# Kernel tuning notes

Hardware: AMD Instinct MI355X
Metric: run time of the kernel (lower is better)

The kernel has to match this reference:

```python
import jax, jax.numpy as jnp
import numpy as np


def setup_inputs() -> dict:
    key = jax.random.key(0)
    k1, k2, k3 = jax.random.split(key, 3)
    B, T, J, D = 32, 2048, 512, 256
    context = jax.random.normal(k1, (B, T, D), dtype=jnp.float32)
    question = jax.random.normal(k2, (B, J, D), dtype=jnp.float32)
    kernel = jax.random.normal(k3, (3 * D, 1), dtype=jnp.float32) * 0.05
    return {"context": context, "question": question, "kernel": kernel}


def reference(context, question, kernel):
    # Original: tile context to (B,T,J,d), question to (B,T,J,d), concat with
    # elementwise product -> (B,T,J,3d), dot with kernel (3d,1), squeeze.
    # Algebraically identical decomposition (kernel = [wc; wq; wm]):
    #   S[b,t,j] = c[b,t]@wc + q[b,j]@wq + (c[b,t]*wm)@q[b,j]
    D = context.shape[-1]
    w = jnp.squeeze(kernel, axis=-1)          # (3d,)
    wc, wq, wm = w[:D], w[D:2 * D], w[2 * D:]
    c_term = context @ wc                     # (B, T)
    q_term = question @ wq                    # (B, J)
    cross = jnp.einsum('btd,bjd->btj', context * wm, question)  # (B, T, J)
    return cross + c_term[:, :, None] + q_term[:, None, :]
```

## Files before the change

kernel.cpp:

```cpp
#include <hip/hip_runtime.h>
#include <stdint.h>

typedef __bf16 bf16x8 __attribute__((ext_vector_type(8)));
typedef float  f32x4  __attribute__((ext_vector_type(4)));

typedef __attribute__((address_space(1))) const void g_void;
typedef __attribute__((address_space(3))) void l_void;

constexpr int NB = 32, TT = 2048, JJ = 512, DD = 256;
constexpr int CTX_ROWS = NB * TT;
constexpr int QUE_ROWS = NB * JJ;

constexpr size_t WS_QUEB  = 33554432;
constexpr size_t WS_CTERM = 41943040;
constexpr size_t WS_QTERM = 42205184;
constexpr size_t WS_NEED  = 42270720;

__global__ __launch_bounds__(256)
void prep_kernel(const float* __restrict__ ctx, const float* __restrict__ que,
                 const float* __restrict__ wvec,
                 __bf16* __restrict__ ctxb, __bf16* __restrict__ queb,
                 float* __restrict__ cterm, float* __restrict__ qterm)
{
    const int tid  = threadIdx.x;
    const int colg = tid & 31;
    const int rloc = tid >> 5;
    const int k0   = colg * 8;

    const bool isC = (blockIdx.x < 2048);
    const float* src0  = isC ? ctx  : que;
    __bf16*      dst0  = isC ? ctxb : queb;
    float*       term0 = isC ? cterm : qterm;
    const int    rows   = isC ? CTX_ROWS : QUE_ROWS;
    const int    stride = isC ? 2048 * 8 : 512 * 8;
    const int    rg0    = isC ? blockIdx.x : blockIdx.x - 2048;

    const f32x4 wd0 = *(const f32x4*)(wvec + (isC ? 0 : DD) + k0);
    const f32x4 wd1 = *(const f32x4*)(wvec + (isC ? 0 : DD) + k0 + 4);
    f32x4 wm0 = {1.f, 1.f, 1.f, 1.f}, wm1 = {1.f, 1.f, 1.f, 1.f};
    if (isC) { wm0 = *(const f32x4*)(wvec + 2 * DD + k0);
               wm1 = *(const f32x4*)(wvec + 2 * DD + k0 + 4); }

    for (int r = rg0 * 8 + rloc; r < rows; r += stride) {
        const float* src = src0 + (size_t)r * DD + k0;
        const f32x4 x0 = *(const f32x4*)src;
        const f32x4 x1 = *(const f32x4*)(src + 4);

        float d = x0[0]*wd0[0] + x0[1]*wd0[1] + x0[2]*wd0[2] + x0[3]*wd0[3]
                + x1[0]*wd1[0] + x1[1]*wd1[1] + x1[2]*wd1[2] + x1[3]*wd1[3];
        d += __shfl_xor(d, 1);  d += __shfl_xor(d, 2);  d += __shfl_xor(d, 4);
        d += __shfl_xor(d, 8);  d += __shfl_xor(d, 16);

        bf16x8 pk;
        #pragma unroll
        for (int j = 0; j < 4; ++j) {
            pk[j]     = (__bf16)(x0[j] * wm0[j]);
            pk[4 + j] = (__bf16)(x1[j] * wm1[j]);
        }
        *(bf16x8*)(dst0 + (size_t)r * DD + k0) = pk;
        if (colg == 0) term0[r] = d;
    }
}

__global__ __launch_bounds__(256)
void gemm_kernel(const __bf16* __restrict__ ctxb, const __bf16* __restrict__ queb,
                 const float* __restrict__ cterm, const float* __restrict__ qterm,
                 float* __restrict__ out)
{
    __shared__ __align__(1024) unsigned char lds[32768];

    const int tid = threadIdx.x;
    const int l   = tid & 63;
    const int wid = tid >> 6;

    const int pb = blockIdx.x;
    const int id = (pb & 7) * 256 + (pb >> 3);
    const int n0 = (id & 3) * 128;
    const int m0 = ((id >> 2) & 15) * 128;
    const int bI = id >> 6;

    const int lrow8 = l >> 3;
    const int lslot = l & 7;
    const int srcsw = (lslot ^ lrow8) << 3;

    const __bf16* aBase = ctxb + ((size_t)bI * TT + m0 + wid * 32 + lrow8) * DD + srcsw;
    const __bf16* bBase = queb + ((size_t)bI * JJ + n0 + wid * 32 + lrow8) * DD + srcsw;
    unsigned char* ldsA = lds + wid * 4096;
    unsigned char* ldsB = lds + 16384 + wid * 4096;

    auto stage = [&](int k) {
        #pragma unroll
        for (int j = 0; j < 4; ++j) {
            __builtin_amdgcn_global_load_lds((g_void*)(aBase + (size_t)j * 8 * DD + k * 64),
                                             (l_void*)(ldsA + j * 1024), 16, 0, 0);
            __builtin_amdgcn_global_load_lds((g_void*)(bBase + (size_t)j * 8 * DD + k * 64),
                                             (l_void*)(ldsB + j * 1024), 16, 0, 0);
        }
    };

    stage(0);

    f32x4 acc[4][4];
    #pragma unroll
    for (int m = 0; m < 4; ++m)
        #pragma unroll
        for (int n = 0; n < 4; ++n) acc[m][n] = f32x4{0.f, 0.f, 0.f, 0.f};

    const int wm_0 = (wid >> 1) * 64;
    const int wn_0 = (wid & 1) * 64;
    const int lr = l & 15;
    const int hi = l >> 4;

    #pragma unroll
    for (int k = 0; k < 4; ++k) {
        asm volatile("s_waitcnt vmcnt(0)" ::: "memory");
        __builtin_amdgcn_s_barrier();

        bf16x8 af[2][4], bfr[2][4];
        #pragma unroll
        for (int kk = 0; kk < 2; ++kk) {
            const int c = kk * 4 + hi;
            #pragma unroll
            for (int m = 0; m < 4; ++m) {
                const int r = wm_0 + m * 16 + lr;
                af[kk][m] = *(const bf16x8*)(lds + r * 128 + ((c ^ (r & 7)) << 4));
            }
            #pragma unroll
            for (int n = 0; n < 4; ++n) {
                const int r = wn_0 + n * 16 + lr;
                bfr[kk][n] = *(const bf16x8*)(lds + 16384 + r * 128 + ((c ^ (r & 7)) << 4));
            }
        }
        asm volatile("s_waitcnt lgkmcnt(0)" ::: "memory");
        __builtin_amdgcn_sched_barrier(0);
        __builtin_amdgcn_s_barrier();
        if (k < 3) stage(k + 1);

        __builtin_amdgcn_s_setprio(1);
        #pragma unroll
        for (int kk = 0; kk < 2; ++kk)
            #pragma unroll
            for (int m = 0; m < 4; ++m)
                #pragma unroll
                for (int n = 0; n < 4; ++n)
                    acc[m][n] = __builtin_amdgcn_mfma_f32_16x16x32_bf16(bfr[kk][n], af[kk][m],
                                                                        acc[m][n], 0, 0, 0);
        __builtin_amdgcn_s_setprio(0);
    }

    const int jb = wn_0 + hi * 4;
    #pragma unroll
    for (int m = 0; m < 4; ++m) {
        const int rowL = wm_0 + m * 16 + lr;
        const float cv = cterm[(size_t)bI * TT + m0 + rowL];
        float* rowp = out + ((size_t)bI * TT + m0 + rowL) * JJ + n0;
        #pragma unroll
        for (int n = 0; n < 4; ++n) {
            const int colL = jb + n * 16;
            const f32x4 qv = *(const f32x4*)(qterm + (size_t)bI * JJ + n0 + colL);
            const f32x4 v = acc[m][n];
            f32x4 w = {v[0] + cv + qv[0], v[1] + cv + qv[1],
                       v[2] + cv + qv[2], v[3] + cv + qv[3]};
            *(f32x4*)(rowp + colL) = w;
        }
    }
}

__global__ __launch_bounds__(256)
void naive_kernel(const float* __restrict__ ctx, const float* __restrict__ que,
                  const float* __restrict__ wvec, float* __restrict__ out)
{
    const int j = blockIdx.x * 16 + (threadIdx.x & 15);
    const int t = blockIdx.y * 16 + (threadIdx.x >> 4);
    const int b = blockIdx.z;
    const float* cr = ctx + ((size_t)b * TT + t) * DD;
    const float* qr = que + ((size_t)b * JJ + j) * DD;
    float s = 0.f, ct = 0.f, qt = 0.f;
    for (int k = 0; k < DD; ++k) {
        const float cv = cr[k], qv = qr[k];
        s  += cv * wvec[2 * DD + k] * qv;
        ct += cv * wvec[k];
        qt += qv * wvec[DD + k];
    }
    out[((size_t)b * TT + t) * JJ + j] = s + ct + qt;
}

extern "C" void kernel_launch(void* const* d_in, const int* in_sizes, int n_in,
                              void* d_out, int out_size, void* d_ws, size_t ws_size,
                              hipStream_t stream) {
    (void)in_sizes; (void)n_in; (void)out_size;
    const float* ctx = (const float*)d_in[0];
    const float* que = (const float*)d_in[1];
    const float* wv  = (const float*)d_in[2];
    float* out = (float*)d_out;

    if (ws_size < WS_NEED) {
        naive_kernel<<<dim3(JJ / 16, TT / 16, NB), dim3(256), 0, stream>>>(ctx, que, wv, out);
        return;
    }

    __bf16* ctxb = (__bf16*)d_ws;
    __bf16* queb = (__bf16*)((char*)d_ws + WS_QUEB);
    float*  cterm = (float*)((char*)d_ws + WS_CTERM);
    float*  qterm = (float*)((char*)d_ws + WS_QTERM);

    prep_kernel<<<dim3(2560), dim3(256), 0, stream>>>(ctx, que, wv, ctxb, queb, cterm, qterm);
    gemm_kernel<<<dim3(2048), dim3(256), 0, stream>>>(ctxb, queb, cterm, qterm, out);
}
```

Measured before the change: 62.01 us.

## Double-buffer GEMM LDS staging with K=32 slices and two-deep prefetch

The GEMM main loop now uses 8 K-steps of 32 instead of 4 steps of 64. Two LDS buffers keep two stages in flight, and the loop waits with vmcnt(4) rather than draining all loads. The swizzle is reworked for 64-byte rows. This is meant to hide global-to-LDS latency behind MFMA work, at the cost of more barriers and smaller compute chunks per iteration.

```diff
diff --git a/kernel.cpp b/kernel.cpp
--- a/kernel.cpp
+++ b/kernel.cpp
@@ -79,26 +79,25 @@
     const int m0 = ((id >> 2) & 15) * 128;
     const int bI = id >> 6;
 
-    const int lrow8 = l >> 3;
-    const int lslot = l & 7;
-    const int srcsw = (lslot ^ lrow8) << 3;
-
-    const __bf16* aBase = ctxb + ((size_t)bI * TT + m0 + wid * 32 + lrow8) * DD + srcsw;
-    const __bf16* bBase = queb + ((size_t)bI * JJ + n0 + wid * 32 + lrow8) * DD + srcsw;
-    unsigned char* ldsA = lds + wid * 4096;
-    unsigned char* ldsB = lds + 16384 + wid * 4096;
-
-    auto stage = [&](int k) {
-        #pragma unroll
-        for (int j = 0; j < 4; ++j) {
-            __builtin_amdgcn_global_load_lds((g_void*)(aBase + (size_t)j * 8 * DD + k * 64),
-                                             (l_void*)(ldsA + j * 1024), 16, 0, 0);
-            __builtin_amdgcn_global_load_lds((g_void*)(bBase + (size_t)j * 8 * DD + k * 64),
-                                             (l_void*)(ldsB + j * 1024), 16, 0, 0);
+    const int srow  = wid * 16 + (l >> 2);
+    const int schunk = ((l & 3) ^ ((srow >> 1) & 3)) << 3;
+
+    const __bf16* aBase = ctxb + ((size_t)bI * TT + m0 + srow) * DD + schunk;
+    const __bf16* bBase = queb + ((size_t)bI * JJ + n0 + srow) * DD + schunk;
+    unsigned char* ldsW = lds + wid * 1024;
+
+    auto stage = [&](int k, int b) {
+        #pragma unroll
+        for (int j = 0; j < 2; ++j) {
+            __builtin_amdgcn_global_load_lds((g_void*)(aBase + (size_t)j * 64 * DD + k * 32),
+                                             (l_void*)(ldsW + b * 8192 + j * 4096), 16, 0, 0);
+            __builtin_amdgcn_global_load_lds((g_void*)(bBase + (size_t)j * 64 * DD + k * 32),
+                                             (l_void*)(ldsW + 16384 + b * 8192 + j * 4096), 16, 0, 0);
         }
     };
 
-    stage(0);
+    stage(0, 0);
+    stage(1, 1);
 
     f32x4 acc[4][4];
     #pragma unroll
@@ -112,39 +111,37 @@
     const int hi = l >> 4;
 
     #pragma unroll
-    for (int k = 0; k < 4; ++k) {
-        asm volatile("s_waitcnt vmcnt(0)" ::: "memory");
+    for (int k = 0; k < 8; ++k) {
+        if (k < 7) asm volatile("s_waitcnt vmcnt(4)" ::: "memory");
+        else       asm volatile("s_waitcnt vmcnt(0)" ::: "memory");
         __builtin_amdgcn_s_barrier();
 
-        bf16x8 af[2][4], bfr[2][4];
-        #pragma unroll
-        for (int kk = 0; kk < 2; ++kk) {
-            const int c = kk * 4 + hi;
-            #pragma unroll
-            for (int m = 0; m < 4; ++m) {
-                const int r = wm_0 + m * 16 + lr;
-                af[kk][m] = *(const bf16x8*)(lds + r * 128 + ((c ^ (r & 7)) << 4));
-            }
-            #pragma unroll
-            for (int n = 0; n < 4; ++n) {
-                const int r = wn_0 + n * 16 + lr;
-                bfr[kk][n] = *(const bf16x8*)(lds + 16384 + r * 128 + ((c ^ (r & 7)) << 4));
-            }
+        const unsigned char* bA = lds + (k & 1) * 8192;
+        const unsigned char* bB = bA + 16384;
+
+        bf16x8 af[4], bfr[4];
+        #pragma unroll
+        for (int m = 0; m < 4; ++m) {
+            const int r = wm_0 + m * 16 + lr;
+            af[m] = *(const bf16x8*)(bA + r * 64 + ((hi ^ ((r >> 1) & 3)) << 4));
+        }
+        #pragma unroll
+        for (int n = 0; n < 4; ++n) {
+            const int r = wn_0 + n * 16 + lr;
+            bfr[n] = *(const bf16x8*)(bB + r * 64 + ((hi ^ ((r >> 1) & 3)) << 4));
         }
         asm volatile("s_waitcnt lgkmcnt(0)" ::: "memory");
         __builtin_amdgcn_sched_barrier(0);
         __builtin_amdgcn_s_barrier();
-        if (k < 3) stage(k + 1);
+        if (k < 6) stage(k + 2, k & 1);
 
         __builtin_amdgcn_s_setprio(1);
         #pragma unroll
-        for (int kk = 0; kk < 2; ++kk)
+        for (int m = 0; m < 4; ++m)
             #pragma unroll
-            for (int m = 0; m < 4; ++m)
-                #pragma unroll
-                for (int n = 0; n < 4; ++n)
-                    acc[m][n] = __builtin_amdgcn_mfma_f32_16x16x32_bf16(bfr[kk][n], af[kk][m],
-                                                                        acc[m][n], 0, 0, 0);
+            for (int n = 0; n < 4; ++n)
+                acc[m][n] = __builtin_amdgcn_mfma_f32_16x16x32_bf16(bfr[n], af[m],
+                                                                    acc[m][n], 0, 0, 0);
         __builtin_amdgcn_s_setprio(0);
     }
 
```

Result: no change. 61.24 us (-1.2%).

## Fuse context bf16 conversion and c-term into GEMM, double-buffer question tiles

Applied to the files above, without the earlier changes.

The context prep pass goes away. The GEMM kernel now loads fp32 context rows straight into registers, converts them to bf16, and writes them into swizzled LDS. It also accumulates the c-term dot product with wc from a copy of wc kept in LDS. The wm scaling moves to the question side: a smaller prep kernel scales question by wm, converts it to bf16 and computes the q-term. Question tiles become double-buffered in LDS. This removes the 32MB bf16 context round trip through workspace and the separate c-term buffer. The cost is more fp32 context traffic per tile, repeated across the four J tiles, plus conversion work and more LDS use in the hot kernel.

```diff
diff --git a/kernel.cpp b/kernel.cpp
--- a/kernel.cpp
+++ b/kernel.cpp
@@ -8,70 +8,53 @@
 typedef __attribute__((address_space(3))) void l_void;
 
 constexpr int NB = 32, TT = 2048, JJ = 512, DD = 256;
-constexpr int CTX_ROWS = NB * TT;
-constexpr int QUE_ROWS = NB * JJ;
-
-constexpr size_t WS_QUEB  = 33554432;
-constexpr size_t WS_CTERM = 41943040;
-constexpr size_t WS_QTERM = 42205184;
-constexpr size_t WS_NEED  = 42270720;
+
+constexpr size_t WS_QTERM = 8388608;
+constexpr size_t WS_NEED  = 8454144;
 
 __global__ __launch_bounds__(256)
-void prep_kernel(const float* __restrict__ ctx, const float* __restrict__ que,
-                 const float* __restrict__ wvec,
-                 __bf16* __restrict__ ctxb, __bf16* __restrict__ queb,
-                 float* __restrict__ cterm, float* __restrict__ qterm)
+void qprep_kernel(const float* __restrict__ que, const float* __restrict__ wvec,
+                  __bf16* __restrict__ queb, float* __restrict__ qterm)
 {
-    const int tid  = threadIdx.x;
-    const int colg = tid & 31;
-    const int rloc = tid >> 5;
-    const int k0   = colg * 8;
-
-    const bool isC = (blockIdx.x < 2048);
-    const float* src0  = isC ? ctx  : que;
-    __bf16*      dst0  = isC ? ctxb : queb;
-    float*       term0 = isC ? cterm : qterm;
-    const int    rows   = isC ? CTX_ROWS : QUE_ROWS;
-    const int    stride = isC ? 2048 * 8 : 512 * 8;
-    const int    rg0    = isC ? blockIdx.x : blockIdx.x - 2048;
-
-    const f32x4 wd0 = *(const f32x4*)(wvec + (isC ? 0 : DD) + k0);
-    const f32x4 wd1 = *(const f32x4*)(wvec + (isC ? 0 : DD) + k0 + 4);
-    f32x4 wm0 = {1.f, 1.f, 1.f, 1.f}, wm1 = {1.f, 1.f, 1.f, 1.f};
-    if (isC) { wm0 = *(const f32x4*)(wvec + 2 * DD + k0);
-               wm1 = *(const f32x4*)(wvec + 2 * DD + k0 + 4); }
-
-    for (int r = rg0 * 8 + rloc; r < rows; r += stride) {
-        const float* src = src0 + (size_t)r * DD + k0;
+    const int tid = threadIdx.x;
+    const int colg = tid & 31, rloc = tid >> 5;
+    const int k0 = colg * 8;
+    const f32x4 wq0 = *(const f32x4*)(wvec + DD + k0);
+    const f32x4 wq1 = *(const f32x4*)(wvec + DD + k0 + 4);
+    const f32x4 wm0 = *(const f32x4*)(wvec + 2 * DD + k0);
+    const f32x4 wm1 = *(const f32x4*)(wvec + 2 * DD + k0 + 4);
+    #pragma unroll
+    for (int i = 0; i < 4; ++i) {
+        const int r = blockIdx.x * 32 + i * 8 + rloc;
+        const float* src = que + (size_t)r * DD + k0;
         const f32x4 x0 = *(const f32x4*)src;
         const f32x4 x1 = *(const f32x4*)(src + 4);
-
-        float d = x0[0]*wd0[0] + x0[1]*wd0[1] + x0[2]*wd0[2] + x0[3]*wd0[3]
-                + x1[0]*wd1[0] + x1[1]*wd1[1] + x1[2]*wd1[2] + x1[3]*wd1[3];
+        float d = x0[0]*wq0[0] + x0[1]*wq0[1] + x0[2]*wq0[2] + x0[3]*wq0[3]
+                + x1[0]*wq1[0] + x1[1]*wq1[1] + x1[2]*wq1[2] + x1[3]*wq1[3];
         d += __shfl_xor(d, 1);  d += __shfl_xor(d, 2);  d += __shfl_xor(d, 4);
         d += __shfl_xor(d, 8);  d += __shfl_xor(d, 16);
-
         bf16x8 pk;
         #pragma unroll
         for (int j = 0; j < 4; ++j) {
             pk[j]     = (__bf16)(x0[j] * wm0[j]);
             pk[4 + j] = (__bf16)(x1[j] * wm1[j]);
         }
-        *(bf16x8*)(dst0 + (size_t)r * DD + k0) = pk;
-        if (colg == 0) term0[r] = d;
+        *(bf16x8*)(queb + (size_t)r * DD + k0) = pk;
+        if (colg == 0) qterm[r] = d;
     }
 }
 
 __global__ __launch_bounds__(256)
-void gemm_kernel(const __bf16* __restrict__ ctxb, const __bf16* __restrict__ queb,
-                 const float* __restrict__ cterm, const float* __restrict__ qterm,
+void main_kernel(const float* __restrict__ ctx, const float* __restrict__ wvec,
+                 const __bf16* __restrict__ queb, const float* __restrict__ qterm,
                  float* __restrict__ out)
 {
-    __shared__ __align__(1024) unsigned char lds[32768];
+    __shared__ __align__(1024) unsigned char lds[50688];
+    float* wc_s = (float*)(lds + 49152);
+    float* c_s  = (float*)(lds + 50176);
 
     const int tid = threadIdx.x;
-    const int l   = tid & 63;
-    const int wid = tid >> 6;
+    const int l = tid & 63, wid = tid >> 6;
 
     const int pb = blockIdx.x;
     const int id = (pb & 7) * 256 + (pb >> 3);
@@ -79,26 +62,34 @@
     const int m0 = ((id >> 2) & 15) * 128;
     const int bI = id >> 6;
 
-    const int lrow8 = l >> 3;
-    const int lslot = l & 7;
-    const int srcsw = (lslot ^ lrow8) << 3;
-
-    const __bf16* aBase = ctxb + ((size_t)bI * TT + m0 + wid * 32 + lrow8) * DD + srcsw;
-    const __bf16* bBase = queb + ((size_t)bI * JJ + n0 + wid * 32 + lrow8) * DD + srcsw;
-    unsigned char* ldsA = lds + wid * 4096;
-    unsigned char* ldsB = lds + 16384 + wid * 4096;
-
-    auto stage = [&](int k) {
-        #pragma unroll
-        for (int j = 0; j < 4; ++j) {
-            __builtin_amdgcn_global_load_lds((g_void*)(aBase + (size_t)j * 8 * DD + k * 64),
-                                             (l_void*)(ldsA + j * 1024), 16, 0, 0);
-            __builtin_amdgcn_global_load_lds((g_void*)(bBase + (size_t)j * 8 * DD + k * 64),
-                                             (l_void*)(ldsB + j * 1024), 16, 0, 0);
-        }
+    if (tid < 64) *(f32x4*)(wc_s + tid * 4) = *(const f32x4*)(wvec + tid * 4);
+
+    const int arow = tid >> 1, ahalf = tid & 1;
+    const float* aSrc = ctx + ((size_t)bI * TT + m0 + arow) * DD + ahalf * 32;
+
+    const int brow = wid * 32 + (l >> 3);
+    const int bsl  = ((l & 7) ^ ((l >> 3) & 7)) << 3;
+    const __bf16* bSrc = queb + ((size_t)bI * JJ + n0 + brow) * DD + bsl;
+    unsigned char* bDst = lds + 16384 + wid * 4096;
+
+    auto stageB = [&](int k, int buf) {
+        #pragma unroll
+        for (int j = 0; j < 4; ++j)
+            __builtin_amdgcn_global_load_lds((g_void*)(bSrc + (size_t)j * 8 * DD + k * 64),
+                                             (l_void*)(bDst + buf * 16384 + j * 1024), 16, 0, 0);
     };
 
-    stage(0);
+    f32x4 a[8];
+    auto loadA = [&](int k) {
+        #pragma unroll
+        for (int c = 0; c < 8; ++c) a[c] = *(const f32x4*)(aSrc + k * 64 + c * 4);
+    };
+
+    stageB(0, 0);
+    loadA(0);
+    stageB(1, 1);
+    asm volatile("s_waitcnt lgkmcnt(0)" ::: "memory");
+    __builtin_amdgcn_s_barrier();
 
     f32x4 acc[4][4];
     #pragma unroll
@@ -108,15 +99,44 @@
 
     const int wm_0 = (wid >> 1) * 64;
     const int wn_0 = (wid & 1) * 64;
-    const int lr = l & 15;
-    const int hi = l >> 4;
+    const int lr = l & 15, hi = l >> 4;
+
+    float cp = 0.f;
+    unsigned char* aWr = lds + arow * 128;
+    const int asw = arow & 7;
 
     #pragma unroll
     for (int k = 0; k < 4; ++k) {
-        asm volatile("s_waitcnt vmcnt(0)" ::: "memory");
+        bf16x8 pa[4];
+        {
+            const float* wcp = wc_s + k * 64 + ahalf * 32;
+            #pragma unroll
+            for (int c2 = 0; c2 < 4; ++c2) {
+                const f32x4 w0 = *(const f32x4*)(wcp + c2 * 8);
+                const f32x4 w1 = *(const f32x4*)(wcp + c2 * 8 + 4);
+                #pragma unroll
+                for (int j = 0; j < 4; ++j) {
+                    pa[c2][j]     = (__bf16)a[c2 * 2][j];
+                    pa[c2][4 + j] = (__bf16)a[c2 * 2 + 1][j];
+                    cp += a[c2 * 2][j] * w0[j] + a[c2 * 2 + 1][j] * w1[j];
+                }
+            }
+        }
         __builtin_amdgcn_s_barrier();
 
-        bf16x8 af[2][4], bfr[2][4];
+        #pragma unroll
+        for (int c2 = 0; c2 < 4; ++c2)
+            *(bf16x8*)(aWr + (((ahalf * 4 + c2) ^ asw) << 4)) = pa[c2];
+
+        if (k >= 1 && k < 3) stageB(k + 1, (k + 1) & 1);
+        if (k < 3) loadA(k + 1);
+
+        asm volatile("s_waitcnt lgkmcnt(0)" ::: "memory");
+        __builtin_amdgcn_sched_barrier(0);
+        __builtin_amdgcn_s_barrier();
+
+        const unsigned char* bBuf = lds + 16384 + (k & 1) * 16384;
+        bf16x8 af[2][4], bf[2][4];
         #pragma unroll
         for (int kk = 0; kk < 2; ++kk) {
             const int c = kk * 4 + hi;
@@ -128,14 +148,9 @@
             #pragma unroll
             for (int n = 0; n < 4; ++n) {
                 const int r = wn_0 + n * 16 + lr;
-                bfr[kk][n] = *(const bf16x8*)(lds + 16384 + r * 128 + ((c ^ (r & 7)) << 4));
+                bf[kk][n] = *(const bf16x8*)(bBuf + r * 128 + ((c ^ (r & 7)) << 4));
             }
         }
-        asm volatile("s_waitcnt lgkmcnt(0)" ::: "memory");
-        __builtin_amdgcn_sched_barrier(0);
-        __builtin_amdgcn_s_barrier();
-        if (k < 3) stage(k + 1);
-
         __builtin_amdgcn_s_setprio(1);
         #pragma unroll
         for (int kk = 0; kk < 2; ++kk)
@@ -143,16 +158,20 @@
             for (int m = 0; m < 4; ++m)
                 #pragma unroll
                 for (int n = 0; n < 4; ++n)
-                    acc[m][n] = __builtin_amdgcn_mfma_f32_16x16x32_bf16(bfr[kk][n], af[kk][m],
+                    acc[m][n] = __builtin_amdgcn_mfma_f32_16x16x32_bf16(bf[kk][n], af[kk][m],
                                                                         acc[m][n], 0, 0, 0);
         __builtin_amdgcn_s_setprio(0);
     }
 
+    cp += __shfl_xor(cp, 1);
+    if (ahalf == 0) c_s[arow] = cp;
+    __syncthreads();
+
     const int jb = wn_0 + hi * 4;
     #pragma unroll
     for (int m = 0; m < 4; ++m) {
         const int rowL = wm_0 + m * 16 + lr;
-        const float cv = cterm[(size_t)bI * TT + m0 + rowL];
+        const float cv = c_s[rowL];
         float* rowp = out + ((size_t)bI * TT + m0 + rowL) * JJ + n0;
         #pragma unroll
         for (int n = 0; n < 4; ++n) {
@@ -199,11 +218,9 @@
         return;
     }
 
-    __bf16* ctxb = (__bf16*)d_ws;
-    __bf16* queb = (__bf16*)((char*)d_ws + WS_QUEB);
-    float*  cterm = (float*)((char*)d_ws + WS_CTERM);
+    __bf16* queb  = (__bf16*)d_ws;
     float*  qterm = (float*)((char*)d_ws + WS_QTERM);
 
-    prep_kernel<<<dim3(2560), dim3(256), 0, stream>>>(ctx, que, wv, ctxb, queb, cterm, qterm);
-    gemm_kernel<<<dim3(2048), dim3(256), 0, stream>>>(ctxb, queb, cterm, qterm, out);
-}
+    qprep_kernel<<<dim3(512), dim3(256), 0, stream>>>(que, wv, queb, qterm);
+    main_kernel<<<dim3(2048), dim3(256), 0, stream>>>(ctx, wv, queb, qterm, out);
+}
```

Result: slower. 71.79 us (+15.8%).
